# Kernel optimization log

Hardware: AMD Instinct MI355X
Metric: run time of the kernel (lower is better)

Reference implementation:

```python
import jax, jax.numpy as jnp
import numpy as np

H, C = 4, 32          # num_heads, hidden_channels
NEG_ATT = 0.2         # GAT attention leaky_relu slope (PyG default)
NEG_ACT = 0.01        # F.leaky_relu default slope applied after each conv


def gat_conv(x_src, x_dst, Wsrc, Wdst, a_src, a_dst, bias, src_idx, dst_idx, n_dst):
    """One bipartite GATConv (add_self_loops=False, concat=True)."""
    hs = (x_src @ Wsrc).reshape(-1, H, C)            # [Ns,H,C]
    hd = (x_dst @ Wdst).reshape(-1, H, C)            # [Nd,H,C]
    a_s = (hs * a_src).sum(-1)                       # [Ns,H]
    a_d = (hd * a_dst).sum(-1)                       # [Nd,H]
    e = jax.nn.leaky_relu(a_s[src_idx] + a_d[dst_idx], NEG_ATT)  # [E,H]
    m = jax.ops.segment_max(e, dst_idx, num_segments=n_dst)      # [Nd,H]
    ex = jnp.exp(e - m[dst_idx])
    denom = jax.ops.segment_sum(ex, dst_idx, num_segments=n_dst)
    alpha = ex / (denom[dst_idx] + 1e-16)            # edge softmax over dst
    msg = hs[src_idx] * alpha[:, :, None]            # [E,H,C]
    out = jax.ops.segment_sum(msg, dst_idx, num_segments=n_dst)  # [Nd,H,C]
    return out.reshape(n_dst, H * C) + bias


def setup_inputs() -> dict:
    key = jax.random.key(0)
    ks = jax.random.split(key, 40)
    it = iter(range(40))
    Nu, Nm, E, D, O = 100000, 20000, 500000, 64, 64
    HC = H * C

    def rn(shape, s=0.1):
        return jax.random.normal(ks[next(it)], shape, jnp.float32) * s

    def ri(n, hi):
        return jax.random.randint(ks[next(it)], (n,), 0, hi)

    return {
        "user_ids": jnp.arange(Nu), "movie_ids": jnp.arange(Nm),
        "um_src": ri(E, Nu), "um_dst": ri(E, Nm),
        "mu_src": ri(E, Nm), "mu_dst": ri(E, Nu),
        "user_emb": rn((Nu, D)), "movie_emb": rn((Nm, D)),
        "l1_um_Wsrc": rn((D, HC)), "l1_um_Wdst": rn((D, HC)),
        "l1_um_asrc": rn((H, C)), "l1_um_adst": rn((H, C)), "l1_um_b": rn((HC,)),
        "l1_mu_Wsrc": rn((D, HC)), "l1_mu_Wdst": rn((D, HC)),
        "l1_mu_asrc": rn((H, C)), "l1_mu_adst": rn((H, C)), "l1_mu_b": rn((HC,)),
        "l2_um_W": rn((HC, HC)), "l2_um_asrc": rn((H, C)), "l2_um_adst": rn((H, C)), "l2_um_b": rn((HC,)),
        "l2_mu_W": rn((HC, HC)), "l2_mu_asrc": rn((H, C)), "l2_mu_adst": rn((H, C)), "l2_mu_b": rn((HC,)),
        "Wo": rn((HC, O)), "bo": rn((O,)),
    }


def reference(user_ids, movie_ids, um_src, um_dst, mu_src, mu_dst,
              user_emb, movie_emb,
              l1_um_Wsrc, l1_um_Wdst, l1_um_asrc, l1_um_adst, l1_um_b,
              l1_mu_Wsrc, l1_mu_Wdst, l1_mu_asrc, l1_mu_adst, l1_mu_b,
              l2_um_W, l2_um_asrc, l2_um_adst, l2_um_b,
              l2_mu_W, l2_mu_asrc, l2_mu_adst, l2_mu_b,
              Wo, bo):
    xu = user_emb[user_ids]
    xm = movie_emb[movie_ids]
    Nu, Nm = xu.shape[0], xm.shape[0]
    # layer 1 (HeteroConv sum: each dst type receives exactly one edge type here)
    hm = gat_conv(xu, xm, l1_um_Wsrc, l1_um_Wdst, l1_um_asrc, l1_um_adst, l1_um_b, um_src, um_dst, Nm)
    hu = gat_conv(xm, xu, l1_mu_Wsrc, l1_mu_Wdst, l1_mu_asrc, l1_mu_adst, l1_mu_b, mu_src, mu_dst, Nu)
    xu = jax.nn.leaky_relu(hu, NEG_ACT)
    xm = jax.nn.leaky_relu(hm, NEG_ACT)
    # layer 2 (non-bipartite in_channels int => shared lin for src and dst)
    hm = gat_conv(xu, xm, l2_um_W, l2_um_W, l2_um_asrc, l2_um_adst, l2_um_b, um_src, um_dst, Nm)
    hu = gat_conv(xm, xu, l2_mu_W, l2_mu_W, l2_mu_asrc, l2_mu_adst, l2_mu_b, mu_src, mu_dst, Nu)
    xu = jax.nn.leaky_relu(hu, NEG_ACT)
    xm = jax.nn.leaky_relu(hm, NEG_ACT)
    out_user = xu @ Wo + bo
    out_movie = xm @ Wo + bo
    return out_user, out_movie, xu, xm
```

## Files before the change

### kernel.cpp

```cpp
#include <hip/hip_runtime.h>
#include <hip/hip_bf16.h>
#include <cstdint>


#define HC 128
#define HH 4
#define NWIN 4

typedef __attribute__((ext_vector_type(8))) short bf16x8;
typedef __attribute__((ext_vector_type(4))) float f32x4;

__device__ __forceinline__ short f2bf(float f) {
    return __builtin_bit_cast(short, __float2bfloat16(f));
}
__device__ __forceinline__ float bf2f(ushort u) {
    return __builtin_bit_cast(float, ((unsigned)u) << 16);
}

struct VT { const float* W[8]; const float* a[8]; float* v[8]; };
__global__ void make_v_all_k(VT t) {
    int gid = blockIdx.x * 256 + threadIdx.x;
    int task, base;
    if (gid < 1024) { task = gid >> 8; base = gid & 255; }
    else if (gid < 3072) { int g = gid - 1024; task = 4 + (g >> 9); base = g & 511; }
    else return;
    int k = base >> 2, h = base & 3;
    int coff = (task & 1) * 4;
    const float* wr = t.W[task] + (size_t)k * HC + h * 32;
    const float* ar = t.a[task] + h * 32;
    float s = 0.f;
    #pragma unroll
    for (int c = 0; c < 32; ++c) s = fmaf(wr[c], ar[c], s);
    t.v[task][k * 8 + coff + h] = s;
}

struct PT { const float* W[5]; const float* V[5]; ushort* Wb[5];
            int K[5]; int Nw[5]; int start[6]; };
__global__ void pack_all_k(PT t) {
    int gid = blockIdx.x * 256 + threadIdx.x;
    if (gid >= t.start[5]) return;
    int task = 0;
    while (gid >= t.start[task + 1]) ++task;
    int loc = gid - t.start[task];
    int K = t.K[task], Nw = t.Nw[task];
    int n = loc / K, k = loc % K;
    float v = 0.f;
    if (n < Nw) v = t.W[task][(size_t)k * Nw + n];
    else if (t.V[task] != nullptr && n < Nw + 8) v = t.V[task][k * 8 + (n - Nw)];
    t.Wb[task][loc] = (ushort)f2bf(v);
}

template <int NT, int MODE, bool ABF>
__global__ __launch_bounds__(256) void gemm_dual_k(
    const void* A0, const int* idx0, const ushort* Wb0, ushort* hsb0,
    float* atts0, float* attd0, float* C0, const float* bias0, int M0, int nb0,
    const void* A1, const int* idx1, const ushort* Wb1, ushort* hsb1,
    float* atts1, float* attd1, float* C1, const float* bias1, int M1,
    int K, int ldc) {
    const void* A; const int* aidx; const ushort* Wb; ushort* hsb;
    float* atts; float* attd; float* C; const float* bias; int M, bid;
    if ((int)blockIdx.x < nb0) {
        A = A0; aidx = idx0; Wb = Wb0; hsb = hsb0; atts = atts0; attd = attd0;
        C = C0; bias = bias0; M = M0; bid = blockIdx.x;
    } else {
        A = A1; aidx = idx1; Wb = Wb1; hsb = hsb1; atts = atts1; attd = attd1;
        C = C1; bias = bias1; M = M1; bid = blockIdx.x - nb0;
    }
    int lane = threadIdx.x & 63;
    int wave = threadIdx.x >> 6;
    int m_base = bid * 128 + wave * 32;
    int lm = lane & 15;
    int kg = lane >> 4;

    int r0 = m_base + lm, r1 = r0 + 16;
    int cr0 = r0 < M ? r0 : M - 1;
    int cr1 = r1 < M ? r1 : M - 1;
    int row0 = aidx ? aidx[cr0] : cr0;
    int row1 = aidx ? aidx[cr1] : cr1;
    const ushort* bp = Wb + (size_t)lm * K + kg * 8;

    f32x4 acc[2][NT] = {};
    for (int k0 = 0; k0 < K; k0 += 32) {
        bf16x8 a[2];
        if (ABF) {
            const ushort* a0p = (const ushort*)A + (size_t)row0 * K + kg * 8;
            const ushort* a1p = (const ushort*)A + (size_t)row1 * K + kg * 8;
            a[0] = *reinterpret_cast<const bf16x8*>(a0p + k0);
            a[1] = *reinterpret_cast<const bf16x8*>(a1p + k0);
        } else {
            const float* a0p = (const float*)A + (size_t)row0 * K + kg * 8;
            const float* a1p = (const float*)A + (size_t)row1 * K + kg * 8;
            float af[2][8];
            *reinterpret_cast<float4*>(&af[0][0]) = *reinterpret_cast<const float4*>(a0p + k0);
            *reinterpret_cast<float4*>(&af[0][4]) = *reinterpret_cast<const float4*>(a0p + k0 + 4);
            *reinterpret_cast<float4*>(&af[1][0]) = *reinterpret_cast<const float4*>(a1p + k0);
            *reinterpret_cast<float4*>(&af[1][4]) = *reinterpret_cast<const float4*>(a1p + k0 + 4);
            #pragma unroll
            for (int mi = 0; mi < 2; ++mi)
                #pragma unroll
                for (int j = 0; j < 8; ++j) a[mi][j] = f2bf(af[mi][j]);
        }
        #pragma unroll
        for (int nt = 0; nt < NT; ++nt) {
            bf16x8 b = *reinterpret_cast<const bf16x8*>(bp + (size_t)nt * 16 * K + k0);
            acc[0][nt] = __builtin_amdgcn_mfma_f32_16x16x32_bf16(a[0], b, acc[0][nt], 0, 0, 0);
            acc[1][nt] = __builtin_amdgcn_mfma_f32_16x16x32_bf16(a[1], b, acc[1][nt], 0, 0, 0);
        }
    }
    #pragma unroll
    for (int mi = 0; mi < 2; ++mi) {
        int rowb = m_base + mi * 16 + kg * 4;
        if (MODE == 0) {
            #pragma unroll
            for (int nt = 0; nt < NT - 1; ++nt) {
                int col = nt * 16 + lm;
                #pragma unroll
                for (int r = 0; r < 4; ++r) {
                    int row = rowb + r;
                    if (row < M) hsb[(size_t)row * HC + col] = (ushort)f2bf(acc[mi][nt][r]);
                }
            }
            #pragma unroll
            for (int r = 0; r < 4; ++r) {
                int row = rowb + r;
                if (row < M) {
                    float v = acc[mi][NT - 1][r];
                    if (lm < 4) atts[(size_t)row * 4 + lm] = v;
                    else if (lm < 8) attd[(size_t)row * 4 + (lm - 4)] = v;
                }
            }
        } else {
            #pragma unroll
            for (int nt = 0; nt < NT; ++nt) {
                int col = nt * 16 + lm;
                float bv = bias[col];
                #pragma unroll
                for (int r = 0; r < 4; ++r) {
                    int row = rowb + r;
                    if (row < M) C[(size_t)row * ldc + col] = acc[mi][nt][r] + bv;
                }
            }
        }
    }
}

__global__ void hist_dual_k(const int* __restrict__ d0, int* __restrict__ c0, int E0,
                            const int* __restrict__ d1, int* __restrict__ c1, int E1,
                            int* __restrict__ rank) {
    int e = blockIdx.x * 256 + threadIdx.x;
    if (e < E0) rank[e] = atomicAdd(&c0[d0[e]], 1);
    else if (e - E0 < E1) rank[e] = atomicAdd(&c1[d1[e - E0]], 1);
}

__device__ __forceinline__ void scan_block_body(
    const int* deg, int n, int len, int* out, int* partial, int b) {
    __shared__ int s[256];
    int i = b * 256 + threadIdx.x;
    int v = (i < n) ? deg[i] : 0;
    s[threadIdx.x] = v;
    __syncthreads();
    for (int off = 1; off < 256; off <<= 1) {
        int t = (threadIdx.x >= off) ? s[threadIdx.x - off] : 0;
        __syncthreads();
        s[threadIdx.x] += t;
        __syncthreads();
    }
    if (i < len) out[i] = s[threadIdx.x] - v;
    if (threadIdx.x == 255) partial[b] = s[255];
}

__global__ void scan_block_dual_k(const int* dM, int nM, int* rsM, int* pM, int nbM,
                                  const int* dU, int nU, int* rsU, int* pU) {
    if ((int)blockIdx.x < nbM)
        scan_block_body(dM, nM, nM + 1, rsM, pM, blockIdx.x);
    else
        scan_block_body(dU, nU, nU + 1, rsU, pU, blockIdx.x - nbM);
}

__global__ void scan_partial_dual_k(int* pM, int nbM, int* pU, int nbU) {
    __shared__ int s[512];
    int t = threadIdx.x;
    for (int seg = 0; seg < 2; ++seg) {
        int* p = seg ? pU : pM;
        int nb = seg ? nbU : nbM;
        int v = (t < nb) ? p[t] : 0;
        s[t] = v;
        __syncthreads();
        for (int off = 1; off < 512; off <<= 1) {
            int x = (t >= off) ? s[t - off] : 0;
            __syncthreads();
            s[t] += x;
            __syncthreads();
        }
        if (t < nb) p[t] = s[t] - v;
        __syncthreads();
    }
}

__global__ void add_off_dual_k(int* __restrict__ oM, const int* __restrict__ pM,
                               int lenM, int nbM,
                               int* __restrict__ oU, const int* __restrict__ pU,
                               int lenU) {
    int b = blockIdx.x;
    if (b < nbM) {
        int i = b * 256 + threadIdx.x;
        if (i < lenM) oM[i] += pM[b];
    } else {
        b -= nbM;
        int i = b * 256 + threadIdx.x;
        if (i < lenU) oU[i] += pU[b];
    }
}

__global__ void fill_dual_k(const int* __restrict__ s0, const int* __restrict__ d0,
                            const int* __restrict__ rs0, int* __restrict__ csr0,
                            int E0, int n0,
                            const int* __restrict__ s1, const int* __restrict__ d1,
                            const int* __restrict__ rs1, int* __restrict__ csr1,
                            int E1, int n1,
                            const int* __restrict__ rank) {
    int e = blockIdx.x * 256 + threadIdx.x;
    int w = blockIdx.y;
    if (e < E0) {
        int d = d0[e];
        int lo = (int)((long)w * n0 / NWIN), hi = (int)((long)(w + 1) * n0 / NWIN);
        if (d >= lo && d < hi) csr0[rs0[d] + rank[e]] = s0[e];
    } else if (e - E0 < E1) {
        int e1 = e - E0;
        int d = d1[e1];
        int lo = (int)((long)w * n1 / NWIN), hi = (int)((long)(w + 1) * n1 / NWIN);
        if (d >= lo && d < hi) csr1[rs1[d] + rank[e]] = s1[e1];
    }
}

template <bool WF32, bool WBF>
__global__ __launch_bounds__(256) void agg16_dual_k(
    const int* __restrict__ rs0, const int* __restrict__ csr0,
    const ushort* __restrict__ hsb0, const float* __restrict__ atts0,
    const float* __restrict__ attd0, const float* __restrict__ bias0,
    float* __restrict__ out0, ushort* __restrict__ outb0, int n0,
    const int* __restrict__ rs1, const int* __restrict__ csr1,
    const ushort* __restrict__ hsb1, const float* __restrict__ atts1,
    const float* __restrict__ attd1, const float* __restrict__ bias1,
    float* __restrict__ out1, ushort* __restrict__ outb1, int n1) {
    int g = (int)((blockIdx.x * 256u + threadIdx.x) >> 4);
    const int* rs; const int* csr; const ushort* hsb; const float* atts;
    const float* attd; const float* bias; float* out; ushort* outb; int node;
    if (g < n0) {
        rs = rs0; csr = csr0; hsb = hsb0; atts = atts0; attd = attd0;
        bias = bias0; out = out0; outb = outb0; node = g;
    } else {
        node = g - n0;
        if (node >= n1) return;
        rs = rs1; csr = csr1; hsb = hsb1; atts = atts1; attd = attd1;
        bias = bias1; out = out1; outb = outb1;
    }
    int c = threadIdx.x & 15;
    int h = c >> 2;
    float ad = attd[node * 4 + h];
    int s0 = rs[node], s1 = rs[node + 1];
    float acc[8] = {};
    float wsum = 0.f;
    int i = s0;
    for (; i + 4 <= s1; i += 4) {
        int sx[4];
        #pragma unroll
        for (int j = 0; j < 4; ++j) sx[j] = csr[i + j];
        bf16x8 hv[4]; float el[4];
        #pragma unroll
        for (int j = 0; j < 4; ++j) {
            hv[j] = *reinterpret_cast<const bf16x8*>(hsb + (size_t)sx[j] * HC + 8 * c);
            el[j] = atts[(size_t)sx[j] * 4 + h];
        }
        #pragma unroll
        for (int j = 0; j < 4; ++j) {
            float e = el[j] + ad;
            e = e > 0.f ? e : 0.2f * e;
            float w = __expf(e);
            wsum += w;
            #pragma unroll
            for (int k = 0; k < 8; ++k)
                acc[k] = fmaf(w, bf2f((ushort)hv[j][k]), acc[k]);
        }
    }
    for (; i < s1; ++i) {
        int src = csr[i];
        bf16x8 hv = *reinterpret_cast<const bf16x8*>(hsb + (size_t)src * HC + 8 * c);
        float e = atts[(size_t)src * 4 + h] + ad;
        e = e > 0.f ? e : 0.2f * e;
        float w = __expf(e);
        wsum += w;
        #pragma unroll
        for (int k = 0; k < 8; ++k)
            acc[k] = fmaf(w, bf2f((ushort)hv[k]), acc[k]);
    }
    float inv = 1.f / (wsum + 1e-16f);
    float v[8];
    #pragma unroll
    for (int k = 0; k < 8; ++k) {
        v[k] = fmaf(acc[k], inv, bias[8 * c + k]);
        v[k] = v[k] > 0.f ? v[k] : 0.01f * v[k];
    }
    if (WF32) {
        float4 o0 = make_float4(v[0], v[1], v[2], v[3]);
        float4 o1 = make_float4(v[4], v[5], v[6], v[7]);
        reinterpret_cast<float4*>(out + (size_t)node * HC + 8 * c)[0] = o0;
        reinterpret_cast<float4*>(out + (size_t)node * HC + 8 * c)[1] = o1;
    }
    if (WBF) {
        bf16x8 u;
        #pragma unroll
        for (int k = 0; k < 8; ++k) u[k] = f2bf(v[k]);
        *reinterpret_cast<bf16x8*>(outb + (size_t)node * HC + 8 * c) = u;
    }
}

extern "C" void kernel_launch(void* const* d_in, const int* in_sizes, int n_in,
                              void* d_out, int out_size, void* d_ws, size_t ws_size,
                              hipStream_t stream) {
    const int Nu = in_sizes[0];
    const int Nm = in_sizes[1];
    const int E1 = in_sizes[2];
    const int E2 = in_sizes[4];
    const int D  = in_sizes[6] / Nu;
    const int O  = in_sizes[27];

    const int*   user_ids  = (const int*)d_in[0];
    const int*   movie_ids = (const int*)d_in[1];
    const int*   um_src    = (const int*)d_in[2];
    const int*   um_dst    = (const int*)d_in[3];
    const int*   mu_src    = (const int*)d_in[4];
    const int*   mu_dst    = (const int*)d_in[5];
    const float* user_emb  = (const float*)d_in[6];
    const float* movie_emb = (const float*)d_in[7];
    const float* l1_um_Wsrc = (const float*)d_in[8];
    const float* l1_um_Wdst = (const float*)d_in[9];
    const float* l1_um_asrc = (const float*)d_in[10];
    const float* l1_um_adst = (const float*)d_in[11];
    const float* l1_um_b    = (const float*)d_in[12];
    const float* l1_mu_Wsrc = (const float*)d_in[13];
    const float* l1_mu_Wdst = (const float*)d_in[14];
    const float* l1_mu_asrc = (const float*)d_in[15];
    const float* l1_mu_adst = (const float*)d_in[16];
    const float* l1_mu_b    = (const float*)d_in[17];
    const float* l2_um_W    = (const float*)d_in[18];
    const float* l2_um_asrc = (const float*)d_in[19];
    const float* l2_um_adst = (const float*)d_in[20];
    const float* l2_um_b    = (const float*)d_in[21];
    const float* l2_mu_W    = (const float*)d_in[22];
    const float* l2_mu_asrc = (const float*)d_in[23];
    const float* l2_mu_adst = (const float*)d_in[24];
    const float* l2_mu_b    = (const float*)d_in[25];
    const float* Wo         = (const float*)d_in[26];
    const float* bo         = (const float*)d_in[27];

    char* p = (char*)d_ws;
    auto alloc = [&](size_t bytes) { void* r = p; p += (bytes + 255) & ~(size_t)255; return r; };
    ushort* hs_u = (ushort*)alloc((size_t)Nu * HC * 2);
    ushort* hs_m = (ushort*)alloc((size_t)Nm * HC * 2);
    ushort* XUb  = (ushort*)alloc((size_t)Nu * HC * 2);
    ushort* XMb  = (ushort*)alloc((size_t)Nm * HC * 2);
    float* atts_u = (float*)alloc((size_t)Nu * 4 * 4);
    float* attd_u = (float*)alloc((size_t)Nu * 4 * 4);
    float* atts_m = (float*)alloc((size_t)Nm * 4 * 4);
    float* attd_m = (float*)alloc((size_t)Nm * 4 * 4);
    float* V_u1  = (float*)alloc((size_t)HC * 8 * 4);
    float* V_m1  = (float*)alloc((size_t)HC * 8 * 4);
    float* V_u2  = (float*)alloc((size_t)HC * 8 * 4);
    float* V_m2  = (float*)alloc((size_t)HC * 8 * 4);
    ushort* Wb_u1 = (ushort*)alloc((size_t)144 * D * 2);
    ushort* Wb_m1 = (ushort*)alloc((size_t)144 * D * 2);
    ushort* Wb_u2 = (ushort*)alloc((size_t)144 * HC * 2);
    ushort* Wb_m2 = (ushort*)alloc((size_t)144 * HC * 2);
    ushort* Wb_o  = (ushort*)alloc((size_t)64 * HC * 2);
    int* um_rs  = (int*)alloc((size_t)(Nm + 1) * 4);
    int* mu_rs  = (int*)alloc((size_t)(Nu + 1) * 4);
    int* cnts   = (int*)alloc((size_t)(Nm + Nu) * 4);
    int* um_cnt = cnts;
    int* mu_cnt = cnts + Nm;
    int* um_csr = (int*)alloc((size_t)E1 * 4);
    int* mu_csr = (int*)alloc((size_t)E2 * 4);
    int* rank   = (int*)alloc((size_t)(E1 + E2) * 4);
    int* partM  = (int*)alloc(512 * 4);
    int* partU  = (int*)alloc(512 * 4);

    auto cdiv = [](int a, int b) { return (a + b - 1) / b; };

    {
        VT vt;
        const float* Ws[8] = {l1_um_Wsrc, l1_mu_Wdst, l1_mu_Wsrc, l1_um_Wdst,
                              l2_um_W, l2_mu_W, l2_mu_W, l2_um_W};
        const float* as[8] = {l1_um_asrc, l1_mu_adst, l1_mu_asrc, l1_um_adst,
                              l2_um_asrc, l2_mu_adst, l2_mu_asrc, l2_um_adst};
        float* vs[8] = {V_u1, V_u1, V_m1, V_m1, V_u2, V_u2, V_m2, V_m2};
        for (int i = 0; i < 8; ++i) { vt.W[i] = Ws[i]; vt.a[i] = as[i]; vt.v[i] = vs[i]; }
        make_v_all_k<<<12, 256, 0, stream>>>(vt);

        PT pt;
        const float* pW[5] = {l1_um_Wsrc, l1_mu_Wsrc, l2_um_W, l2_mu_W, Wo};
        const float* pV[5] = {V_u1, V_m1, V_u2, V_m2, nullptr};
        ushort* pB[5] = {Wb_u1, Wb_m1, Wb_u2, Wb_m2, Wb_o};
        int pK[5] = {D, D, HC, HC, HC};
        int pN[5] = {HC, HC, HC, HC, 64};
        int cum = 0;
        for (int i = 0; i < 5; ++i) {
            pt.W[i] = pW[i]; pt.V[i] = pV[i]; pt.Wb[i] = pB[i];
            pt.K[i] = pK[i]; pt.Nw[i] = pN[i];
            pt.start[i] = cum;
            cum += (i < 4 ? 144 : 64) * pK[i];
        }
        pt.start[5] = cum;
        pack_all_k<<<cdiv(cum, 256), 256, 0, stream>>>(pt);
    }

    int nbM = cdiv(Nm + 1, 256), nbU = cdiv(Nu + 1, 256);
    hipMemsetAsync(cnts, 0, (size_t)(Nm + Nu) * 4, stream);
    hist_dual_k<<<cdiv(E1 + E2, 256), 256, 0, stream>>>(
        um_dst, um_cnt, E1, mu_dst, mu_cnt, E2, rank);
    scan_block_dual_k<<<nbM + nbU, 256, 0, stream>>>(um_cnt, Nm, um_rs, partM, nbM,
                                                     mu_cnt, Nu, mu_rs, partU);
    scan_partial_dual_k<<<1, 512, 0, stream>>>(partM, nbM, partU, nbU);
    add_off_dual_k<<<nbM + nbU, 256, 0, stream>>>(um_rs, partM, Nm + 1, nbM,
                                                  mu_rs, partU, Nu + 1);
    {
        dim3 g(cdiv(E1 + E2, 256), NWIN);
        fill_dual_k<<<g, 256, 0, stream>>>(
            um_src, um_dst, um_rs, um_csr, E1, Nm,
            mu_src, mu_dst, mu_rs, mu_csr, E2, Nu, rank);
    }

    float* OU = (float*)d_out;
    float* OM = OU + (size_t)Nu * O;
    float* XU = OM + (size_t)Nm * O;
    float* XM = XU + (size_t)Nu * HC;

    int gbU = cdiv(Nu, 128), gbM = cdiv(Nm, 128);
    int aggBlocks = cdiv((Nm + Nu) * 16, 256);

    gemm_dual_k<9, 0, false><<<gbU + gbM, 256, 0, stream>>>(
        user_emb, user_ids, Wb_u1, hs_u, atts_u, attd_u, nullptr, nullptr, Nu, gbU,
        movie_emb, movie_ids, Wb_m1, hs_m, atts_m, attd_m, nullptr, nullptr, Nm,
        D, 0);
    agg16_dual_k<false, true><<<aggBlocks, 256, 0, stream>>>(
        um_rs, um_csr, hs_u, atts_u, attd_m, l1_um_b, nullptr, XMb, Nm,
        mu_rs, mu_csr, hs_m, atts_m, attd_u, l1_mu_b, nullptr, XUb, Nu);

    gemm_dual_k<9, 0, true><<<gbU + gbM, 256, 0, stream>>>(
        XUb, nullptr, Wb_u2, hs_u, atts_u, attd_u, nullptr, nullptr, Nu, gbU,
        XMb, nullptr, Wb_m2, hs_m, atts_m, attd_m, nullptr, nullptr, Nm,
        HC, 0);
    agg16_dual_k<true, false><<<aggBlocks, 256, 0, stream>>>(
        um_rs, um_csr, hs_u, atts_u, attd_m, l2_um_b, XM, nullptr, Nm,
        mu_rs, mu_csr, hs_m, atts_m, attd_u, l2_mu_b, XU, nullptr, Nu);

    gemm_dual_k<4, 1, false><<<gbU + gbM, 256, 0, stream>>>(
        XU, nullptr, Wb_o, nullptr, nullptr, nullptr, OU, bo, Nu, gbU,
        XM, nullptr, Wb_o, nullptr, nullptr, nullptr, OM, bo, Nm,
        HC, O);
}
```

Baseline: 247.8 us.

## Bucket CSR edges by source-index window to improve gather locality in aggregation

Edges are grouped into source-range windows (8 for user->movie, 2 for movie->user) inside the CSR, so the count and row-start arrays grow to windows x nodes. The aggregation kernel walks the windows in order, so concurrent waves tend to gather from the same slice of source features, which is meant to improve cache hit rate. In exchange the histogram, scan and row-start arrays get larger, a 1024-thread partial scan is needed, and each node does more row-start lookups and short tail loops.

```diff
diff --git a/kernel.cpp b/kernel.cpp
--- a/kernel.cpp
+++ b/kernel.cpp
@@ -6,6 +6,8 @@
 #define HC 128
 #define HH 4
 #define NWIN 4
+#define NWM 8
+#define NWU 2
 
 typedef __attribute__((ext_vector_type(8))) short bf16x8;
 typedef __attribute__((ext_vector_type(4))) float f32x4;
@@ -144,12 +146,20 @@
     }
 }
 
-__global__ void hist_dual_k(const int* __restrict__ d0, int* __restrict__ c0, int E0,
-                            const int* __restrict__ d1, int* __restrict__ c1, int E1,
+__global__ void hist_dual_k(const int* __restrict__ s0, const int* __restrict__ d0,
+                            int* __restrict__ c0, int E0, int nsrc0, int n0,
+                            const int* __restrict__ s1, const int* __restrict__ d1,
+                            int* __restrict__ c1, int E1, int nsrc1, int n1,
                             int* __restrict__ rank) {
     int e = blockIdx.x * 256 + threadIdx.x;
-    if (e < E0) rank[e] = atomicAdd(&c0[d0[e]], 1);
-    else if (e - E0 < E1) rank[e] = atomicAdd(&c1[d1[e - E0]], 1);
+    if (e < E0) {
+        int w = (int)((long)s0[e] * NWM / nsrc0);
+        rank[e] = atomicAdd(&c0[w * n0 + d0[e]], 1);
+    } else if (e - E0 < E1) {
+        int e1 = e - E0;
+        int w = (int)((long)s1[e1] * NWU / nsrc1);
+        rank[e] = atomicAdd(&c1[w * n1 + d1[e1]], 1);
+    }
 }
 
 __device__ __forceinline__ void scan_block_body(
@@ -178,7 +188,7 @@
 }
 
 __global__ void scan_partial_dual_k(int* pM, int nbM, int* pU, int nbU) {
-    __shared__ int s[512];
+    __shared__ int s[1024];
     int t = threadIdx.x;
     for (int seg = 0; seg < 2; ++seg) {
         int* p = seg ? pU : pM;
@@ -186,7 +196,7 @@
         int v = (t < nb) ? p[t] : 0;
         s[t] = v;
         __syncthreads();
-        for (int off = 1; off < 512; off <<= 1) {
+        for (int off = 1; off < 1024; off <<= 1) {
             int x = (t >= off) ? s[t - off] : 0;
             __syncthreads();
             s[t] += x;
@@ -214,22 +224,28 @@
 
 __global__ void fill_dual_k(const int* __restrict__ s0, const int* __restrict__ d0,
                             const int* __restrict__ rs0, int* __restrict__ csr0,
-                            int E0, int n0,
+                            int E0, int nsrc0, int n0,
                             const int* __restrict__ s1, const int* __restrict__ d1,
                             const int* __restrict__ rs1, int* __restrict__ csr1,
-                            int E1, int n1,
+                            int E1, int nsrc1, int n1,
                             const int* __restrict__ rank) {
     int e = blockIdx.x * 256 + threadIdx.x;
-    int w = blockIdx.y;
+    int y = blockIdx.y;
     if (e < E0) {
         int d = d0[e];
-        int lo = (int)((long)w * n0 / NWIN), hi = (int)((long)(w + 1) * n0 / NWIN);
-        if (d >= lo && d < hi) csr0[rs0[d] + rank[e]] = s0[e];
+        int lo = (int)((long)y * n0 / NWIN), hi = (int)((long)(y + 1) * n0 / NWIN);
+        if (d >= lo && d < hi) {
+            int w = (int)((long)s0[e] * NWM / nsrc0);
+            csr0[rs0[w * n0 + d] + rank[e]] = s0[e];
+        }
     } else if (e - E0 < E1) {
         int e1 = e - E0;
         int d = d1[e1];
-        int lo = (int)((long)w * n1 / NWIN), hi = (int)((long)(w + 1) * n1 / NWIN);
-        if (d >= lo && d < hi) csr1[rs1[d] + rank[e]] = s1[e1];
+        int lo = (int)((long)y * n1 / NWIN), hi = (int)((long)(y + 1) * n1 / NWIN);
+        if (d >= lo && d < hi) {
+            int w = (int)((long)s1[e1] * NWU / nsrc1);
+            csr1[rs1[w * n1 + d] + rank[e]] = s1[e1];
+        }
     }
 }
 
@@ -245,54 +261,73 @@
     float* __restrict__ out1, ushort* __restrict__ outb1, int n1) {
     int g = (int)((blockIdx.x * 256u + threadIdx.x) >> 4);
     const int* rs; const int* csr; const ushort* hsb; const float* atts;
-    const float* attd; const float* bias; float* out; ushort* outb; int node;
+    const float* attd; const float* bias; float* out; ushort* outb;
+    int node, nn, nw;
     if (g < n0) {
         rs = rs0; csr = csr0; hsb = hsb0; atts = atts0; attd = attd0;
-        bias = bias0; out = out0; outb = outb0; node = g;
+        bias = bias0; out = out0; outb = outb0; node = g; nn = n0; nw = NWM;
     } else {
         node = g - n0;
         if (node >= n1) return;
         rs = rs1; csr = csr1; hsb = hsb1; atts = atts1; attd = attd1;
-        bias = bias1; out = out1; outb = outb1;
+        bias = bias1; out = out1; outb = outb1; nn = n1; nw = NWU;
     }
     int c = threadIdx.x & 15;
     int h = c >> 2;
     float ad = attd[node * 4 + h];
-    int s0 = rs[node], s1 = rs[node + 1];
     float acc[8] = {};
     float wsum = 0.f;
-    int i = s0;
-    for (; i + 4 <= s1; i += 4) {
-        int sx[4];
-        #pragma unroll
-        for (int j = 0; j < 4; ++j) sx[j] = csr[i + j];
-        bf16x8 hv[4]; float el[4];
-        #pragma unroll
-        for (int j = 0; j < 4; ++j) {
-            hv[j] = *reinterpret_cast<const bf16x8*>(hsb + (size_t)sx[j] * HC + 8 * c);
-            el[j] = atts[(size_t)sx[j] * 4 + h];
-        }
-        #pragma unroll
-        for (int j = 0; j < 4; ++j) {
-            float e = el[j] + ad;
+    for (int w = 0; w < nw; ++w) {
+        int s0 = rs[w * nn + node], s1 = rs[w * nn + node + 1];
+        int i = s0;
+        for (; i + 4 <= s1; i += 4) {
+            int sx[4];
+            #pragma unroll
+            for (int j = 0; j < 4; ++j) sx[j] = csr[i + j];
+            bf16x8 hv[4]; float el[4];
+            #pragma unroll
+            for (int j = 0; j < 4; ++j) {
+                hv[j] = *reinterpret_cast<const bf16x8*>(hsb + (size_t)sx[j] * HC + 8 * c);
+                el[j] = atts[(size_t)sx[j] * 4 + h];
+            }
+            #pragma unroll
+            for (int j = 0; j < 4; ++j) {
+                float e = el[j] + ad;
+                e = e > 0.f ? e : 0.2f * e;
+                float wt = __expf(e);
+                wsum += wt;
+                #pragma unroll
+                for (int k = 0; k < 8; ++k)
+                    acc[k] = fmaf(wt, bf2f((ushort)hv[j][k]), acc[k]);
+            }
+        }
+        if (i + 2 <= s1) {
+            int sa = csr[i], sb = csr[i + 1];
+            bf16x8 ha = *reinterpret_cast<const bf16x8*>(hsb + (size_t)sa * HC + 8 * c);
+            bf16x8 hb = *reinterpret_cast<const bf16x8*>(hsb + (size_t)sb * HC + 8 * c);
+            float ea = atts[(size_t)sa * 4 + h] + ad;
+            float eb = atts[(size_t)sb * 4 + h] + ad;
+            ea = ea > 0.f ? ea : 0.2f * ea;
+            eb = eb > 0.f ? eb : 0.2f * eb;
+            float wa = __expf(ea), wb = __expf(eb);
+            wsum += wa + wb;
+            #pragma unroll
+            for (int k = 0; k < 8; ++k)
+                acc[k] = fmaf(wa, bf2f((ushort)ha[k]),
+                              fmaf(wb, bf2f((ushort)hb[k]), acc[k]));
+            i += 2;
+        }
+        if (i < s1) {
+            int src = csr[i];
+            bf16x8 hv = *reinterpret_cast<const bf16x8*>(hsb + (size_t)src * HC + 8 * c);
+            float e = atts[(size_t)src * 4 + h] + ad;
             e = e > 0.f ? e : 0.2f * e;
-            float w = __expf(e);
-            wsum += w;
+            float wt = __expf(e);
+            wsum += wt;
             #pragma unroll
             for (int k = 0; k < 8; ++k)
-                acc[k] = fmaf(w, bf2f((ushort)hv[j][k]), acc[k]);
-        }
-    }
-    for (; i < s1; ++i) {
-        int src = csr[i];
-        bf16x8 hv = *reinterpret_cast<const bf16x8*>(hsb + (size_t)src * HC + 8 * c);
-        float e = atts[(size_t)src * 4 + h] + ad;
-        e = e > 0.f ? e : 0.2f * e;
-        float w = __expf(e);
-        wsum += w;
-        #pragma unroll
-        for (int k = 0; k < 8; ++k)
-            acc[k] = fmaf(w, bf2f((ushort)hv[k]), acc[k]);
+                acc[k] = fmaf(wt, bf2f((ushort)hv[k]), acc[k]);
+        }
     }
     float inv = 1.f / (wsum + 1e-16f);
     float v[8];
@@ -373,16 +408,17 @@
     ushort* Wb_u2 = (ushort*)alloc((size_t)144 * HC * 2);
     ushort* Wb_m2 = (ushort*)alloc((size_t)144 * HC * 2);
     ushort* Wb_o  = (ushort*)alloc((size_t)64 * HC * 2);
-    int* um_rs  = (int*)alloc((size_t)(Nm + 1) * 4);
-    int* mu_rs  = (int*)alloc((size_t)(Nu + 1) * 4);
-    int* cnts   = (int*)alloc((size_t)(Nm + Nu) * 4);
+    int lenM = NWM * Nm + 1, lenU = NWU * Nu + 1;
+    int* um_rs  = (int*)alloc((size_t)lenM * 4);
+    int* mu_rs  = (int*)alloc((size_t)lenU * 4);
+    int* cnts   = (int*)alloc((size_t)(NWM * Nm + NWU * Nu) * 4);
     int* um_cnt = cnts;
-    int* mu_cnt = cnts + Nm;
+    int* mu_cnt = cnts + NWM * Nm;
     int* um_csr = (int*)alloc((size_t)E1 * 4);
     int* mu_csr = (int*)alloc((size_t)E2 * 4);
     int* rank   = (int*)alloc((size_t)(E1 + E2) * 4);
-    int* partM  = (int*)alloc(512 * 4);
-    int* partU  = (int*)alloc(512 * 4);
+    int* partM  = (int*)alloc(1024 * 4);
+    int* partU  = (int*)alloc(1024 * 4);
 
     auto cdiv = [](int a, int b) { return (a + b - 1) / b; };
 
@@ -413,20 +449,22 @@
         pack_all_k<<<cdiv(cum, 256), 256, 0, stream>>>(pt);
     }
 
-    int nbM = cdiv(Nm + 1, 256), nbU = cdiv(Nu + 1, 256);
-    hipMemsetAsync(cnts, 0, (size_t)(Nm + Nu) * 4, stream);
+    int nbM = cdiv(lenM, 256), nbU = cdiv(lenU, 256);
+    hipMemsetAsync(cnts, 0, (size_t)(NWM * Nm + NWU * Nu) * 4, stream);
     hist_dual_k<<<cdiv(E1 + E2, 256), 256, 0, stream>>>(
-        um_dst, um_cnt, E1, mu_dst, mu_cnt, E2, rank);
-    scan_block_dual_k<<<nbM + nbU, 256, 0, stream>>>(um_cnt, Nm, um_rs, partM, nbM,
-                                                     mu_cnt, Nu, mu_rs, partU);
-    scan_partial_dual_k<<<1, 512, 0, stream>>>(partM, nbM, partU, nbU);
-    add_off_dual_k<<<nbM + nbU, 256, 0, stream>>>(um_rs, partM, Nm + 1, nbM,
-                                                  mu_rs, partU, Nu + 1);
+        um_src, um_dst, um_cnt, E1, Nu, Nm,
+        mu_src, mu_dst, mu_cnt, E2, Nm, Nu, rank);
+    scan_block_dual_k<<<nbM + nbU, 256, 0, stream>>>(
+        um_cnt, NWM * Nm, um_rs, partM, nbM,
+        mu_cnt, NWU * Nu, mu_rs, partU);
+    scan_partial_dual_k<<<1, 1024, 0, stream>>>(partM, nbM, partU, nbU);
+    add_off_dual_k<<<nbM + nbU, 256, 0, stream>>>(um_rs, partM, lenM, nbM,
+                                                  mu_rs, partU, lenU);
     {
         dim3 g(cdiv(E1 + E2, 256), NWIN);
         fill_dual_k<<<g, 256, 0, stream>>>(
-            um_src, um_dst, um_rs, um_csr, E1, Nm,
-            mu_src, mu_dst, mu_rs, mu_csr, E2, Nu, rank);
+            um_src, um_dst, um_rs, um_csr, E1, Nu, Nm,
+            mu_src, mu_dst, mu_rs, mu_csr, E2, Nm, Nu, rank);
     }
 
     float* OU = (float*)d_out;
```

After: 253.0 us. +2.1%, slower.
